# Optimization experiments

Hardware: AMD Instinct MI355X
Metric: run time of the kernel (lower is better)

The kernel has to match this reference:

```python
import jax, jax.numpy as jnp
import numpy as np

N = 100000
E = 3200000
CH_IN = 128
HID = 128
CH_OUT = 3


def setup_inputs() -> dict:
    key = jax.random.key(0)
    ks = jax.random.split(key, 16)
    def lin(kw, fan_in, fan_out):
        bound = 1.0 / np.sqrt(fan_in)
        kw1, kw2 = jax.random.split(kw)
        W = jax.random.uniform(kw1, (fan_in, fan_out), jnp.float32, -bound, bound)
        b = jax.random.uniform(kw2, (fan_out,), jnp.float32, -bound, bound)
        return W, b
    x = jax.random.normal(ks[0], (N, CH_IN), jnp.float32)
    edge_index = jax.random.randint(ks[1], (2, E), 0, N, jnp.int64)
    W1, b1 = lin(ks[2], CH_IN, HID)
    W2, b2 = lin(ks[3], HID, HID)
    lw1, lb1 = lin(ks[4], HID, HID)
    lw2, lb2 = lin(ks[5], HID, HID)
    lw3, lb3 = lin(ks[6], HID, HID)
    lw4, lb4 = lin(ks[7], HID, CH_OUT)
    return {"x": x, "edge_index": edge_index,
            "W1": W1, "b1": b1, "W2": W2, "b2": b2,
            "lw1": lw1, "lb1": lb1, "lw2": lw2, "lb2": lb2,
            "lw3": lw3, "lb3": lb3, "lw4": lw4, "lb4": lb4}


def gcn_conv(x, W, b, src, dst, n_nodes):
    xw = x @ W  # [N, H]
    ew = jnp.ones(src.shape[0], x.dtype)
    deg = jax.ops.segment_sum(ew, dst, num_segments=n_nodes) + 2.0  # +2 from improved self-loop
    dinv = jnp.where(deg > 0, jax.lax.rsqrt(deg), 0.0)
    norm = dinv[src] * dinv[dst]  # [E]
    agg = jax.ops.segment_sum(xw[src] * norm[:, None], dst, num_segments=n_nodes)
    # self-loop contribution: weight 2 * dinv[i]^2 * xw[i]
    agg = agg + xw * (2.0 * dinv * dinv)[:, None]
    return agg + b


def reference(x, edge_index, W1, b1, W2, b2, lw1, lb1, lw2, lb2, lw3, lb3, lw4, lb4):
    src, dst = edge_index[0], edge_index[1]
    n = x.shape[0]
    h = jnp.tanh(gcn_conv(x, W1, b1, src, dst, n))
    h = jnp.tanh(gcn_conv(h, W2, b2, src, dst, n))
    # dropout in eval mode = identity
    h = jnp.tanh(h @ lw1 + lb1)
    h = jnp.tanh(h @ lw2 + lb2)
    h = jnp.tanh(h @ lw3 + lb3)
    return h @ lw4 + lb4
```

## Files before the change

### kernel.cpp

```cpp
#include <hip/hip_runtime.h>

typedef __attribute__((ext_vector_type(8))) short short8;
typedef __attribute__((ext_vector_type(4))) float floatx4;
typedef __attribute__((ext_vector_type(4))) unsigned int uintx4;
typedef unsigned int uint32;

__device__ inline float b2f(unsigned short u) {
    union { uint32 i; float f; } x; x.i = ((uint32)u) << 16; return x.f;
}
__device__ inline float bl(uint32 v) {
    union { uint32 i; float f; } x; x.i = v << 16; return x.f;
}
__device__ inline float bh(uint32 v) {
    union { uint32 i; float f; } x; x.i = v & 0xffff0000u; return x.f;
}
__device__ inline unsigned short f2b(float f) {
    union { float f; uint32 u; } x; x.f = f;
    uint32 r = x.u + 0x7fffu + ((x.u >> 16) & 1u);
    return (unsigned short)(r >> 16);
}
__device__ inline float fast_tanh(float x) {
    float ax = __builtin_fabsf(x);
    float t = __builtin_amdgcn_exp2f(-2.8853900817779268f * ax);
    float r = (1.0f - t) * __builtin_amdgcn_rcpf(1.0f + t);
    return __builtin_copysignf(r, x);
}


#define CHUNK 8192
#define MAXBK 512

__global__ __launch_bounds__(256) void countb_k(const int* __restrict__ eidx,
                                                uint32* __restrict__ bkt_size, int E) {
    __shared__ uint32 hist[MAXBK];
    int t = threadIdx.x;
    hist[t] = 0; hist[t + 256] = 0;
    __syncthreads();
    int base = blockIdx.x * CHUNK;
    int n = E - base; if (n > CHUNK) n = CHUNK;
    for (int i = t; i < n; i += 256) {
        int d = eidx[E + base + i];
        atomicAdd(&hist[d >> 8], 1u);
    }
    __syncthreads();
    uint32 c0 = hist[t], c1 = hist[t + 256];
    if (c0) atomicAdd(&bkt_size[t], c0);
    if (c1) atomicAdd(&bkt_size[t + 256], c1);
}

__global__ __launch_bounds__(MAXBK) void scanb_k(const uint32* __restrict__ bkt_size,
                                                 uint32* __restrict__ bkt_base,
                                                 uint32* __restrict__ bkt_cur, int nbk) {
    __shared__ uint32 s[MAXBK];
    int t = threadIdx.x;
    uint32 v = (t < nbk) ? bkt_size[t] : 0;
    s[t] = v;
    __syncthreads();
    for (int off = 1; off < MAXBK; off <<= 1) {
        uint32 x = (t >= off) ? s[t - off] : 0;
        __syncthreads();
        s[t] += x;
        __syncthreads();
    }
    uint32 excl = s[t] - v;
    bkt_base[t] = excl;
    bkt_cur[t] = excl;
}

__global__ __launch_bounds__(256) void scatterb_k(const int* __restrict__ eidx,
                                                  uint32* __restrict__ bkt_cur,
                                                  uint32* __restrict__ packed, int E) {
    __shared__ uint32 hist[MAXBK];
    __shared__ uint32 temp[256];
    __shared__ uint32 hsc[MAXBK];
    __shared__ uint32 gbase[MAXBK];
    __shared__ uint32 lcur[MAXBK];
    __shared__ uint32 stage[CHUNK];
    __shared__ unsigned short stgb[CHUNK];
    int t = threadIdx.x;
    int cbase = blockIdx.x * CHUNK;
    int n = E - cbase; if (n > CHUNK) n = CHUNK;

    hist[t] = 0; hist[t + 256] = 0;
    __syncthreads();
    for (int i = t; i < n; i += 256) {
        int d = eidx[E + cbase + i];
        atomicAdd(&hist[d >> 8], 1u);
    }
    __syncthreads();
    uint32 c0 = hist[2 * t], c1 = hist[2 * t + 1];
    temp[t] = c0 + c1;
    __syncthreads();
    for (int off = 1; off < 256; off <<= 1) {
        uint32 x = (t >= off) ? temp[t - off] : 0;
        __syncthreads();
        temp[t] += x;
        __syncthreads();
    }
    uint32 exclp = temp[t] - (c0 + c1);
    hsc[2 * t] = exclp;
    hsc[2 * t + 1] = exclp + c0;
    lcur[2 * t] = exclp;
    lcur[2 * t + 1] = exclp + c0;
    if (c0) gbase[2 * t] = atomicAdd(&bkt_cur[2 * t], c0);
    if (c1) gbase[2 * t + 1] = atomicAdd(&bkt_cur[2 * t + 1], c1);
    __syncthreads();
    for (int i = t; i < n; i += 256) {
        int s = eidx[cbase + i];
        int d = eidx[E + cbase + i];
        int b = d >> 8;
        uint32 pos = atomicAdd(&lcur[b], 1u);
        stage[pos] = ((uint32)s << 8) | (uint32)(d & 255);
        stgb[pos] = (unsigned short)b;
    }
    __syncthreads();
    for (int i = t; i < n; i += 256) {
        int b = stgb[i];
        packed[gbase[b] + (i - hsc[b])] = stage[i];
    }
}

__global__ __launch_bounds__(256) void buildb_k(const uint32* __restrict__ packed,
                                                const uint32* __restrict__ bkt_base,
                                                const uint32* __restrict__ bkt_size,
                                                int* __restrict__ rowp,
                                                float* __restrict__ dinv,
                                                int* __restrict__ csr, int N, int E) {
    __shared__ uint32 cnt[256];
    __shared__ uint32 incl[256];
    __shared__ uint32 cur[256];
    int t = threadIdx.x;
    int b = blockIdx.x;
    uint32 base = bkt_base[b];
    uint32 size = bkt_size[b];
    int node0 = b << 8;

    cnt[t] = 0;
    __syncthreads();
    for (uint32 i = t; i < size; i += 256)
        atomicAdd(&cnt[packed[base + i] & 255u], 1u);
    __syncthreads();
    uint32 v = cnt[t];
    incl[t] = v;
    __syncthreads();
    for (int off = 1; off < 256; off <<= 1) {
        uint32 x = (t >= off) ? incl[t - off] : 0;
        __syncthreads();
        incl[t] += x;
        __syncthreads();
    }
    uint32 loc = incl[t] - v;
    cur[t] = loc;
    int node = node0 + t;
    if (node < N) {
        dinv[node] = rsqrtf((float)v + 2.0f);
        rowp[node] = (int)(base + loc);
        if (node == N - 1) rowp[N] = E;
    }
    __syncthreads();
    for (uint32 i = t; i < size; i += 256) {
        uint32 p = packed[base + i];
        uint32 pos = atomicAdd(&cur[p & 255u], 1u);
        csr[base + pos] = (int)(p >> 8);
    }
}


__global__ __launch_bounds__(256) void prep_w5_k(const float* __restrict__ w0,
                                                 const float* __restrict__ w1,
                                                 const float* __restrict__ w2,
                                                 const float* __restrict__ w3,
                                                 const float* __restrict__ w4,
                                                 unsigned short* __restrict__ Wt_hi,
                                                 unsigned short* __restrict__ Wt_lo) {
    int t = blockIdx.x * 256 + threadIdx.x;
    int widx = t >> 11;
    int f8 = t & 2047;
    const float* W;
    switch (widx) {
        case 0: W = w0; break;
        case 1: W = w1; break;
        case 2: W = w2; break;
        case 3: W = w3; break;
        default: W = w4; break;
    }
    int ct = f8 >> 8, kc = (f8 >> 6) & 3, quad = (f8 >> 4) & 3, r = f8 & 15;
    int c = ct * 16 + r;
    int kbase = kc * 32 + quad * 8;
    short8 hi8, lo8;
#pragma unroll
    for (int j = 0; j < 8; ++j) {
        float w = W[(kbase + j) * 128 + c];
        unsigned short h = f2b(w);
        hi8[j] = (short)h;
        lo8[j] = (short)f2b(w - b2f(h));
    }
    *(short8*)(Wt_hi + widx * 16384 + f8 * 8) = hi8;
    *(short8*)(Wt_lo + widx * 16384 + f8 * 8) = lo8;
}


template <int ASRC>
__global__ __launch_bounds__(256, 4) void gemm_z_k(
    const void* __restrict__ Asrc,
    const unsigned short* __restrict__ Wt_hi,
    const unsigned short* __restrict__ Wt_lo,
    const float* __restrict__ dinv,
    unsigned short* __restrict__ out, int N) {
    int tid = threadIdx.x;
    int wave = tid >> 6, lane = tid & 63;
    int quad = lane >> 4, r = lane & 15;
    int m32 = blockIdx.x * 128 + wave * 32;

    short8 af[2][4];
#pragma unroll
    for (int s = 0; s < 2; ++s) {
        int rowA = m32 + s * 16 + r;
        if (rowA >= N) rowA = N - 1;
        if (ASRC == 0) {
            const float4* Af = (const float4*)Asrc;
#pragma unroll
            for (int kc = 0; kc < 4; ++kc) {
                float4 p0 = Af[((size_t)rowA * 128 + kc * 32 + quad * 8) >> 2];
                float4 p1 = Af[(((size_t)rowA * 128 + kc * 32 + quad * 8) >> 2) + 1];
                short8 a;
                a[0] = (short)f2b(p0.x); a[1] = (short)f2b(p0.y);
                a[2] = (short)f2b(p0.z); a[3] = (short)f2b(p0.w);
                a[4] = (short)f2b(p1.x); a[5] = (short)f2b(p1.y);
                a[6] = (short)f2b(p1.z); a[7] = (short)f2b(p1.w);
                af[s][kc] = a;
            }
        } else {
            const short* Ap = (const short*)Asrc;
#pragma unroll
            for (int kc = 0; kc < 4; ++kc)
                af[s][kc] = *(const short8*)(Ap + (size_t)rowA * 128 + kc * 32 + quad * 8);
        }
    }

    float dv[2][4];
#pragma unroll
    for (int s = 0; s < 2; ++s)
#pragma unroll
        for (int reg = 0; reg < 4; ++reg) {
            int i = m32 + s * 16 + quad * 4 + reg;
            dv[s][reg] = dinv[i < N ? i : N - 1];
        }

    const short8* WhF = (const short8*)Wt_hi + lane;
    const short8* WlF = (const short8*)Wt_lo + lane;

#pragma unroll
    for (int ct = 0; ct < 8; ++ct) {
        int n = ct * 16 + r;
        floatx4 a0 = {0.f, 0.f, 0.f, 0.f}, a1 = {0.f, 0.f, 0.f, 0.f};
#pragma unroll
        for (int kc = 0; kc < 4; ++kc) {
            short8 bh8 = WhF[(ct * 4 + kc) << 6];
            a0 = __builtin_amdgcn_mfma_f32_16x16x32_bf16(af[0][kc], bh8, a0, 0, 0, 0);
            a1 = __builtin_amdgcn_mfma_f32_16x16x32_bf16(af[1][kc], bh8, a1, 0, 0, 0);
            short8 bl8 = WlF[(ct * 4 + kc) << 6];
            a0 = __builtin_amdgcn_mfma_f32_16x16x32_bf16(af[0][kc], bl8, a0, 0, 0, 0);
            a1 = __builtin_amdgcn_mfma_f32_16x16x32_bf16(af[1][kc], bl8, a1, 0, 0, 0);
        }
#pragma unroll
        for (int reg = 0; reg < 4; ++reg) {
            int i0 = m32 + quad * 4 + reg;
            if (i0 < N) out[(size_t)i0 * 128 + n] = f2b(a0[reg] * dv[0][reg]);
            int i1 = m32 + 16 + quad * 4 + reg;
            if (i1 < N) out[(size_t)i1 * 128 + n] = f2b(a1[reg] * dv[1][reg]);
        }
    }
}


#define LSTR 136

__global__ __launch_bounds__(256, 1) void mlp_fused_k(
    const unsigned short* __restrict__ H,
    const unsigned short* __restrict__ WH,
    const unsigned short* __restrict__ WL,
    const float* __restrict__ lb1, const float* __restrict__ lb2,
    const float* __restrict__ lb3,
    const float* __restrict__ W4, const float* __restrict__ b4,
    float* __restrict__ out, int N) {
    __shared__ __align__(16) unsigned short wbuf[32768];
    __shared__ __align__(16) unsigned short tile[4][32 * LSTR];
    __shared__ float w4s[384];
    int tid = threadIdx.x;
    if (tid < 192) { w4s[tid] = W4[tid]; w4s[tid + 192] = W4[tid + 192]; }

    int wave = tid >> 6, lane = tid & 63;
    int quad = lane >> 4, r = lane & 15;
    unsigned short* T = tile[wave];
    int m32 = blockIdx.x * 128 + wave * 32;

    short8 af[2][4];
    const short* Hp = (const short*)H;
#pragma unroll
    for (int s = 0; s < 2; ++s) {
        int rowA = m32 + s * 16 + r;
        if (rowA >= N) rowA = N - 1;
#pragma unroll
        for (int kc = 0; kc < 4; ++kc)
            af[s][kc] = *(const short8*)(Hp + (size_t)rowA * 128 + kc * 32 + quad * 8);
    }

    const float* biases[3] = {lb1, lb2, lb3};
#pragma unroll
    for (int L = 0; L < 3; ++L) {
        __syncthreads();
        {
            const uintx4* sh = (const uintx4*)(WH + L * 16384);
            const uintx4* sl = (const uintx4*)(WL + L * 16384);
            uintx4* dh = (uintx4*)wbuf;
            uintx4* dl = (uintx4*)(wbuf + 16384);
#pragma unroll
            for (int it = 0; it < 8; ++it) dh[tid + it * 256] = sh[tid + it * 256];
#pragma unroll
            for (int it = 0; it < 8; ++it) dl[tid + it * 256] = sl[tid + it * 256];
        }
        __syncthreads();
        const float* bias = biases[L];
        float bvv[8];
#pragma unroll
        for (int ct = 0; ct < 8; ++ct) bvv[ct] = bias[ct * 16 + r];
        const short8* whF = (const short8*)wbuf + lane;
        const short8* wlF = (const short8*)(wbuf + 16384) + lane;
#pragma unroll
        for (int ct = 0; ct < 8; ++ct) {
            int n = ct * 16 + r;
            floatx4 a0 = {0.f, 0.f, 0.f, 0.f}, a1 = {0.f, 0.f, 0.f, 0.f};
#pragma unroll
            for (int kc = 0; kc < 4; ++kc) {
                short8 bh8 = whF[(ct * 4 + kc) << 6];
                a0 = __builtin_amdgcn_mfma_f32_16x16x32_bf16(af[0][kc], bh8, a0, 0, 0, 0);
                a1 = __builtin_amdgcn_mfma_f32_16x16x32_bf16(af[1][kc], bh8, a1, 0, 0, 0);
                short8 bl8 = wlF[(ct * 4 + kc) << 6];
                a0 = __builtin_amdgcn_mfma_f32_16x16x32_bf16(af[0][kc], bl8, a0, 0, 0, 0);
                a1 = __builtin_amdgcn_mfma_f32_16x16x32_bf16(af[1][kc], bl8, a1, 0, 0, 0);
            }
            float bv = bvv[ct];
#pragma unroll
            for (int reg = 0; reg < 4; ++reg) {
                int lrow = quad * 4 + reg;
                T[lrow * LSTR + n] = f2b(fast_tanh(a0[reg] + bv));
                T[(lrow + 16) * LSTR + n] = f2b(fast_tanh(a1[reg] + bv));
            }
        }
        if (L < 2) {
#pragma unroll
            for (int s = 0; s < 2; ++s)
#pragma unroll
                for (int kc = 0; kc < 4; ++kc)
                    af[s][kc] = *(const short8*)&T[(s * 16 + r) * LSTR + kc * 32 + quad * 8];
        }
    }

    int lrow = lane & 31;
    int halfc = lane >> 5;
    float a0 = 0.f, a1 = 0.f, a2 = 0.f;
#pragma unroll
    for (int c8 = 0; c8 < 8; ++c8) {
        int cbase = halfc * 64 + c8 * 8;
        short8 hv = *(const short8*)&T[lrow * LSTR + cbase];
#pragma unroll
        for (int j = 0; j < 8; ++j) {
            float xv = b2f((unsigned short)hv[j]);
            int ch = cbase + j;
            a0 = fmaf(xv, w4s[ch * 3 + 0], a0);
            a1 = fmaf(xv, w4s[ch * 3 + 1], a1);
            a2 = fmaf(xv, w4s[ch * 3 + 2], a2);
        }
    }
    a0 += __shfl_xor(a0, 32);
    a1 += __shfl_xor(a1, 32);
    a2 += __shfl_xor(a2, 32);
    if (halfc == 0) {
        int i = m32 + lrow;
        if (i < N) {
            out[(size_t)i * 3 + 0] = a0 + b4[0];
            out[(size_t)i * 3 + 1] = a1 + b4[1];
            out[(size_t)i * 3 + 2] = a2 + b4[2];
        }
    }
}


__global__ __launch_bounds__(256) void agg_half_k(
    const uint32* __restrict__ z, const int* __restrict__ rowp,
    const int* __restrict__ csr, const float* __restrict__ dinv,
    const float* __restrict__ bias, uint32* __restrict__ out, int N, int zoff) {
    int lane = threadIdx.x & 63;
    int half = lane >> 5;
    int c4 = lane & 31;
    int i = blockIdx.x * 4 + (threadIdx.x >> 6);
    if (i >= N) return;
    int start = rowp[i], end = rowp[i + 1];
    const uint32* zh = z + zoff + c4;
    float a0 = 0.f, a1 = 0.f;
    for (int e = start; e < end; e += 64) {
        int cnt = end - e;
        if (cnt > 64) cnt = 64;
        int s = (lane < cnt) ? csr[e + lane] : N;
        int mp = (cnt + 15) & ~15;
        for (int m = 0; m < mp; m += 16) {
            uint32 v[8];
#pragma unroll
            for (int p = 0; p < 8; ++p) {
                int sj = __shfl(s, m + 2 * p + half);
                v[p] = zh[(size_t)sj << 6];
            }
#pragma unroll
            for (int p = 0; p < 8; ++p) {
                a0 += bl(v[p]);
                a1 += bh(v[p]);
            }
        }
    }
    a0 += __shfl_xor(a0, 32);
    a1 += __shfl_xor(a1, 32);
    if (half == 0) {
        uint32 vi = zh[(size_t)i << 6];
        a0 += 2.f * bl(vi);
        a1 += 2.f * bh(vi);
        float di = dinv[i];
        float2 bv = ((const float2*)bias)[zoff + c4];
        float h0 = fast_tanh(fmaf(di, a0, bv.x));
        float h1 = fast_tanh(fmaf(di, a1, bv.y));
        out[((size_t)i << 6) + zoff + c4] = (uint32)f2b(h0) | ((uint32)f2b(h1) << 16);
    }
}

extern "C" void kernel_launch(void* const* d_in, const int* in_sizes, int n_in,
                              void* d_out, int out_size, void* d_ws, size_t ws_size,
                              hipStream_t stream) {
    const float* x   = (const float*)d_in[0];
    const int* eidx  = (const int*)d_in[1];
    const float* W1  = (const float*)d_in[2];
    const float* b1  = (const float*)d_in[3];
    const float* W2  = (const float*)d_in[4];
    const float* b2  = (const float*)d_in[5];
    const float* lw1 = (const float*)d_in[6];
    const float* lb1 = (const float*)d_in[7];
    const float* lw2 = (const float*)d_in[8];
    const float* lb2 = (const float*)d_in[9];
    const float* lw3 = (const float*)d_in[10];
    const float* lb3 = (const float*)d_in[11];
    const float* lw4 = (const float*)d_in[12];
    const float* lb4 = (const float*)d_in[13];
    float* out = (float*)d_out;

    const int N = in_sizes[0] / 128;
    const int E = in_sizes[1] / 2;

    char* p = (char*)d_ws;
    auto alloc = [&](size_t bytes) -> void* {
        void* q = (void*)p;
        p += (bytes + 255) & ~(size_t)255;
        return q;
    };
    float* dinv      = (float*)alloc((size_t)N * 4);
    int* rowp        = (int*)alloc((size_t)(N + 1) * 4);
    uint32* bkt_size = (uint32*)alloc(MAXBK * 4);
    uint32* bkt_base = (uint32*)alloc(MAXBK * 4);
    uint32* bkt_cur  = (uint32*)alloc(MAXBK * 4);
    int* csr         = (int*)alloc((size_t)E * 4);
    unsigned short* Wt_hi = (unsigned short*)alloc(5 * 16384 * 2);
    unsigned short* Wt_lo = (unsigned short*)alloc(5 * 16384 * 2);
    unsigned short* bufA  = (unsigned short*)alloc((size_t)(N + 1) * 128 * 2);
    unsigned short* bufB  = (unsigned short*)alloc((size_t)(N + 1) * 128 * 2);
    uint32* packed = (uint32*)bufA;

    const int MB4 = (N + 127) / 128;
    const int AB  = (N + 3) / 4;
    const int NCH = (E + CHUNK - 1) / CHUNK;
    const int NBK = (N + 255) >> 8;

    hipMemsetAsync(bufA + (size_t)N * 128, 0, 256, stream);
    hipMemsetAsync(bkt_size, 0, MAXBK * 4, stream);
    countb_k<<<NCH, 256, 0, stream>>>(eidx, bkt_size, E);
    prep_w5_k<<<40, 256, 0, stream>>>(W1, W2, lw1, lw2, lw3, Wt_hi, Wt_lo);
    scanb_k<<<1, MAXBK, 0, stream>>>(bkt_size, bkt_base, bkt_cur, NBK);
    scatterb_k<<<NCH, 256, 0, stream>>>(eidx, bkt_cur, packed, E);
    buildb_k<<<NBK, 256, 0, stream>>>(packed, bkt_base, bkt_size, rowp, dinv, csr, N, E);

    const unsigned short* WH = Wt_hi;
    const unsigned short* WL = Wt_lo;

    gemm_z_k<0><<<MB4, 256, 0, stream>>>(x, WH + 0 * 16384, WL + 0 * 16384, dinv, bufA, N);
    agg_half_k<<<AB, 256, 0, stream>>>((const uint32*)bufA, rowp, csr, dinv, b1,
                                       (uint32*)bufB, N, 0);
    agg_half_k<<<AB, 256, 0, stream>>>((const uint32*)bufA, rowp, csr, dinv, b1,
                                       (uint32*)bufB, N, 32);
    gemm_z_k<1><<<MB4, 256, 0, stream>>>(bufB, WH + 1 * 16384, WL + 1 * 16384, dinv, bufA, N);
    agg_half_k<<<AB, 256, 0, stream>>>((const uint32*)bufA, rowp, csr, dinv, b2,
                                       (uint32*)bufB, N, 0);
    agg_half_k<<<AB, 256, 0, stream>>>((const uint32*)bufA, rowp, csr, dinv, b2,
                                       (uint32*)bufB, N, 32);
    mlp_fused_k<<<MB4, 256, 0, stream>>>(bufB, WH + 2 * 16384, WL + 2 * 16384,
                                         lb1, lb2, lb3, lw4, lb4, out, N);
}
```

Measured before the change: 497.1 us.

## Use fixed-capacity edge buckets and halve MLP weight staging for two blocks per CU

New measurement: 470.4 us. 1.06x faster.

```diff
diff --git a/kernel.cpp b/kernel.cpp
--- a/kernel.cpp
+++ b/kernel.cpp
@@ -29,43 +29,7 @@
 
 #define CHUNK 8192
 #define MAXBK 512
-
-__global__ __launch_bounds__(256) void countb_k(const int* __restrict__ eidx,
-                                                uint32* __restrict__ bkt_size, int E) {
-    __shared__ uint32 hist[MAXBK];
-    int t = threadIdx.x;
-    hist[t] = 0; hist[t + 256] = 0;
-    __syncthreads();
-    int base = blockIdx.x * CHUNK;
-    int n = E - base; if (n > CHUNK) n = CHUNK;
-    for (int i = t; i < n; i += 256) {
-        int d = eidx[E + base + i];
-        atomicAdd(&hist[d >> 8], 1u);
-    }
-    __syncthreads();
-    uint32 c0 = hist[t], c1 = hist[t + 256];
-    if (c0) atomicAdd(&bkt_size[t], c0);
-    if (c1) atomicAdd(&bkt_size[t + 256], c1);
-}
-
-__global__ __launch_bounds__(MAXBK) void scanb_k(const uint32* __restrict__ bkt_size,
-                                                 uint32* __restrict__ bkt_base,
-                                                 uint32* __restrict__ bkt_cur, int nbk) {
-    __shared__ uint32 s[MAXBK];
-    int t = threadIdx.x;
-    uint32 v = (t < nbk) ? bkt_size[t] : 0;
-    s[t] = v;
-    __syncthreads();
-    for (int off = 1; off < MAXBK; off <<= 1) {
-        uint32 x = (t >= off) ? s[t - off] : 0;
-        __syncthreads();
-        s[t] += x;
-        __syncthreads();
-    }
-    uint32 excl = s[t] - v;
-    bkt_base[t] = excl;
-    bkt_cur[t] = excl;
-}
+#define CAP   8704
 
 __global__ __launch_bounds__(256) void scatterb_k(const int* __restrict__ eidx,
                                                   uint32* __restrict__ bkt_cur,
@@ -121,18 +85,18 @@
 }
 
 __global__ __launch_bounds__(256) void buildb_k(const uint32* __restrict__ packed,
-                                                const uint32* __restrict__ bkt_base,
-                                                const uint32* __restrict__ bkt_size,
+                                                const uint32* __restrict__ bkt_cur,
                                                 int* __restrict__ rowp,
+                                                int* __restrict__ rowe,
                                                 float* __restrict__ dinv,
-                                                int* __restrict__ csr, int N, int E) {
+                                                int* __restrict__ csr, int N) {
     __shared__ uint32 cnt[256];
     __shared__ uint32 incl[256];
     __shared__ uint32 cur[256];
     int t = threadIdx.x;
     int b = blockIdx.x;
-    uint32 base = bkt_base[b];
-    uint32 size = bkt_size[b];
+    uint32 base = (uint32)b * CAP;
+    uint32 size = bkt_cur[b] - base;
     int node0 = b << 8;
 
     cnt[t] = 0;
@@ -155,7 +119,7 @@
     if (node < N) {
         dinv[node] = rsqrtf((float)v + 2.0f);
         rowp[node] = (int)(base + loc);
-        if (node == N - 1) rowp[N] = E;
+        rowe[node] = (int)(base + loc + v);
     }
     __syncthreads();
     for (uint32 i = t; i < size; i += 256) {
@@ -172,7 +136,12 @@
                                                  const float* __restrict__ w3,
                                                  const float* __restrict__ w4,
                                                  unsigned short* __restrict__ Wt_hi,
-                                                 unsigned short* __restrict__ Wt_lo) {
+                                                 unsigned short* __restrict__ Wt_lo,
+                                                 uint32* __restrict__ bkt_cur) {
+    if (blockIdx.x < 2) {
+        int idx = blockIdx.x * 256 + threadIdx.x;
+        bkt_cur[idx] = (uint32)idx * CAP;
+    }
     int t = blockIdx.x * 256 + threadIdx.x;
     int widx = t >> 11;
     int f8 = t & 2047;
@@ -276,7 +245,7 @@
 
 #define LSTR 136
 
-__global__ __launch_bounds__(256, 1) void mlp_fused_k(
+__global__ __launch_bounds__(256, 2) void mlp_fused_k(
     const unsigned short* __restrict__ H,
     const unsigned short* __restrict__ WH,
     const unsigned short* __restrict__ WL,
@@ -284,7 +253,7 @@
     const float* __restrict__ lb3,
     const float* __restrict__ W4, const float* __restrict__ b4,
     float* __restrict__ out, int N) {
-    __shared__ __align__(16) unsigned short wbuf[32768];
+    __shared__ __align__(16) unsigned short wbuf[16384];
     __shared__ __align__(16) unsigned short tile[4][32 * LSTR];
     __shared__ float w4s[384];
     int tid = threadIdx.x;
@@ -309,43 +278,47 @@
     const float* biases[3] = {lb1, lb2, lb3};
 #pragma unroll
     for (int L = 0; L < 3; ++L) {
-        __syncthreads();
-        {
-            const uintx4* sh = (const uintx4*)(WH + L * 16384);
-            const uintx4* sl = (const uintx4*)(WL + L * 16384);
-            uintx4* dh = (uintx4*)wbuf;
-            uintx4* dl = (uintx4*)(wbuf + 16384);
-#pragma unroll
-            for (int it = 0; it < 8; ++it) dh[tid + it * 256] = sh[tid + it * 256];
-#pragma unroll
-            for (int it = 0; it < 8; ++it) dl[tid + it * 256] = sl[tid + it * 256];
-        }
-        __syncthreads();
         const float* bias = biases[L];
         float bvv[8];
 #pragma unroll
         for (int ct = 0; ct < 8; ++ct) bvv[ct] = bias[ct * 16 + r];
-        const short8* whF = (const short8*)wbuf + lane;
-        const short8* wlF = (const short8*)(wbuf + 16384) + lane;
-#pragma unroll
-        for (int ct = 0; ct < 8; ++ct) {
-            int n = ct * 16 + r;
-            floatx4 a0 = {0.f, 0.f, 0.f, 0.f}, a1 = {0.f, 0.f, 0.f, 0.f};
-#pragma unroll
-            for (int kc = 0; kc < 4; ++kc) {
-                short8 bh8 = whF[(ct * 4 + kc) << 6];
-                a0 = __builtin_amdgcn_mfma_f32_16x16x32_bf16(af[0][kc], bh8, a0, 0, 0, 0);
-                a1 = __builtin_amdgcn_mfma_f32_16x16x32_bf16(af[1][kc], bh8, a1, 0, 0, 0);
-                short8 bl8 = wlF[(ct * 4 + kc) << 6];
-                a0 = __builtin_amdgcn_mfma_f32_16x16x32_bf16(af[0][kc], bl8, a0, 0, 0, 0);
-                a1 = __builtin_amdgcn_mfma_f32_16x16x32_bf16(af[1][kc], bl8, a1, 0, 0, 0);
+#pragma unroll
+        for (int hf = 0; hf < 2; ++hf) {
+            __syncthreads();
+            {
+                const uintx4* sh = (const uintx4*)(WH + L * 16384 + hf * 8192);
+                const uintx4* sl = (const uintx4*)(WL + L * 16384 + hf * 8192);
+                uintx4* dh = (uintx4*)wbuf;
+                uintx4* dl = (uintx4*)(wbuf + 8192);
+#pragma unroll
+                for (int it = 0; it < 4; ++it) dh[tid + it * 256] = sh[tid + it * 256];
+#pragma unroll
+                for (int it = 0; it < 4; ++it) dl[tid + it * 256] = sl[tid + it * 256];
             }
-            float bv = bvv[ct];
-#pragma unroll
-            for (int reg = 0; reg < 4; ++reg) {
-                int lrow = quad * 4 + reg;
-                T[lrow * LSTR + n] = f2b(fast_tanh(a0[reg] + bv));
-                T[(lrow + 16) * LSTR + n] = f2b(fast_tanh(a1[reg] + bv));
+            __syncthreads();
+            const short8* whF = (const short8*)wbuf + lane;
+            const short8* wlF = (const short8*)(wbuf + 8192) + lane;
+#pragma unroll
+            for (int c2 = 0; c2 < 4; ++c2) {
+                int ct = hf * 4 + c2;
+                int n = ct * 16 + r;
+                floatx4 a0 = {0.f, 0.f, 0.f, 0.f}, a1 = {0.f, 0.f, 0.f, 0.f};
+#pragma unroll
+                for (int kc = 0; kc < 4; ++kc) {
+                    short8 bh8 = whF[(c2 * 4 + kc) << 6];
+                    a0 = __builtin_amdgcn_mfma_f32_16x16x32_bf16(af[0][kc], bh8, a0, 0, 0, 0);
+                    a1 = __builtin_amdgcn_mfma_f32_16x16x32_bf16(af[1][kc], bh8, a1, 0, 0, 0);
+                    short8 bl8 = wlF[(c2 * 4 + kc) << 6];
+                    a0 = __builtin_amdgcn_mfma_f32_16x16x32_bf16(af[0][kc], bl8, a0, 0, 0, 0);
+                    a1 = __builtin_amdgcn_mfma_f32_16x16x32_bf16(af[1][kc], bl8, a1, 0, 0, 0);
+                }
+                float bv = bvv[ct];
+#pragma unroll
+                for (int reg = 0; reg < 4; ++reg) {
+                    int lrow = quad * 4 + reg;
+                    T[lrow * LSTR + n] = f2b(fast_tanh(a0[reg] + bv));
+                    T[(lrow + 16) * LSTR + n] = f2b(fast_tanh(a1[reg] + bv));
+                }
             }
         }
         if (L < 2) {
@@ -389,14 +362,15 @@
 
 __global__ __launch_bounds__(256) void agg_half_k(
     const uint32* __restrict__ z, const int* __restrict__ rowp,
-    const int* __restrict__ csr, const float* __restrict__ dinv,
-    const float* __restrict__ bias, uint32* __restrict__ out, int N, int zoff) {
+    const int* __restrict__ rowe, const int* __restrict__ csr,
+    const float* __restrict__ dinv, const float* __restrict__ bias,
+    uint32* __restrict__ out, int N, int zoff) {
     int lane = threadIdx.x & 63;
     int half = lane >> 5;
     int c4 = lane & 31;
     int i = blockIdx.x * 4 + (threadIdx.x >> 6);
     if (i >= N) return;
-    int start = rowp[i], end = rowp[i + 1];
+    int start = rowp[i], end = rowe[i];
     const uint32* zh = z + zoff + c4;
     float a0 = 0.f, a1 = 0.f;
     for (int e = start; e < end; e += 64) {
@@ -460,12 +434,12 @@
         p += (bytes + 255) & ~(size_t)255;
         return q;
     };
+    const int NBK = (N + 255) >> 8;
     float* dinv      = (float*)alloc((size_t)N * 4);
-    int* rowp        = (int*)alloc((size_t)(N + 1) * 4);
-    uint32* bkt_size = (uint32*)alloc(MAXBK * 4);
-    uint32* bkt_base = (uint32*)alloc(MAXBK * 4);
+    int* rowp        = (int*)alloc((size_t)N * 4);
+    int* rowe        = (int*)alloc((size_t)N * 4);
     uint32* bkt_cur  = (uint32*)alloc(MAXBK * 4);
-    int* csr         = (int*)alloc((size_t)E * 4);
+    int* csr         = (int*)alloc((size_t)NBK * CAP * 4);
     unsigned short* Wt_hi = (unsigned short*)alloc(5 * 16384 * 2);
     unsigned short* Wt_lo = (unsigned short*)alloc(5 * 16384 * 2);
     unsigned short* bufA  = (unsigned short*)alloc((size_t)(N + 1) * 128 * 2);
@@ -475,28 +449,24 @@
     const int MB4 = (N + 127) / 128;
     const int AB  = (N + 3) / 4;
     const int NCH = (E + CHUNK - 1) / CHUNK;
-    const int NBK = (N + 255) >> 8;
 
     hipMemsetAsync(bufA + (size_t)N * 128, 0, 256, stream);
-    hipMemsetAsync(bkt_size, 0, MAXBK * 4, stream);
-    countb_k<<<NCH, 256, 0, stream>>>(eidx, bkt_size, E);
-    prep_w5_k<<<40, 256, 0, stream>>>(W1, W2, lw1, lw2, lw3, Wt_hi, Wt_lo);
-    scanb_k<<<1, MAXBK, 0, stream>>>(bkt_size, bkt_base, bkt_cur, NBK);
+    prep_w5_k<<<40, 256, 0, stream>>>(W1, W2, lw1, lw2, lw3, Wt_hi, Wt_lo, bkt_cur);
     scatterb_k<<<NCH, 256, 0, stream>>>(eidx, bkt_cur, packed, E);
-    buildb_k<<<NBK, 256, 0, stream>>>(packed, bkt_base, bkt_size, rowp, dinv, csr, N, E);
+    buildb_k<<<NBK, 256, 0, stream>>>(packed, bkt_cur, rowp, rowe, dinv, csr, N);
 
     const unsigned short* WH = Wt_hi;
     const unsigned short* WL = Wt_lo;
 
     gemm_z_k<0><<<MB4, 256, 0, stream>>>(x, WH + 0 * 16384, WL + 0 * 16384, dinv, bufA, N);
-    agg_half_k<<<AB, 256, 0, stream>>>((const uint32*)bufA, rowp, csr, dinv, b1,
+    agg_half_k<<<AB, 256, 0, stream>>>((const uint32*)bufA, rowp, rowe, csr, dinv, b1,
                                        (uint32*)bufB, N, 0);
-    agg_half_k<<<AB, 256, 0, stream>>>((const uint32*)bufA, rowp, csr, dinv, b1,
+    agg_half_k<<<AB, 256, 0, stream>>>((const uint32*)bufA, rowp, rowe, csr, dinv, b1,
                                        (uint32*)bufB, N, 32);
     gemm_z_k<1><<<MB4, 256, 0, stream>>>(bufB, WH + 1 * 16384, WL + 1 * 16384, dinv, bufA, N);
-    agg_half_k<<<AB, 256, 0, stream>>>((const uint32*)bufA, rowp, csr, dinv, b2,
+    agg_half_k<<<AB, 256, 0, stream>>>((const uint32*)bufA, rowp, rowe, csr, dinv, b2,
                                        (uint32*)bufB, N, 0);
-    agg_half_k<<<AB, 256, 0, stream>>>((const uint32*)bufA, rowp, csr, dinv, b2,
+    agg_half_k<<<AB, 256, 0, stream>>>((const uint32*)bufA, rowp, rowe, csr, dinv, b2,
                                        (uint32*)bufB, N, 32);
     mlp_fused_k<<<MB4, 256, 0, stream>>>(bufB, WH + 2 * 16384, WL + 2 * 16384,
                                          lb1, lb2, lb3, lw4, lb4, out, N);
```
